# Optimization experiments

Measured on AMD Instinct MI355X. Metric: run time of the kernel, lower is better.

Reference implementation:

```python
import jax, jax.numpy as jnp
import numpy as np
from jax import lax

EPS = 1e-5
NBITS_W = 4
NBITS_A = 4
HIDDEN = 192


def _ste(x, q):
    # straight-through estimator: forward q, backward identity
    return x + lax.stop_gradient(q - x)


def act_q(x, bit, signed):
    # ACT_Q: per-tensor uniform activation quantization with max-abs scale (STE)
    if bit >= 32:
        return x
    n = float(2 ** (bit - 1) - 1) if signed else float(2 ** bit - 1)
    scale = lax.stop_gradient(jnp.max(jnp.abs(x)) + 1e-8)
    lo = -1.0 if signed else 0.0
    xc = jnp.clip(x / scale, lo, 1.0)
    q = jnp.round(xc * n) / n * scale
    return _ste(x, q)


def weight_q(w, bit):
    # Conv2d_quan_cim weight quant: symmetric per-tensor max-abs uniform quant (STE)
    if bit >= 32:
        return w
    n = float(2 ** (bit - 1) - 1)
    scale = lax.stop_gradient(jnp.max(jnp.abs(w)) + 1e-8)
    q = jnp.round(jnp.clip(w / scale, -1.0, 1.0) * n) / n * scale
    return _ste(w, q)


def bn(x, g, b, m, v):
    # eval-mode BatchNorm2d over NCHW
    inv = lax.rsqrt(v + EPS)
    return (x - m[None, :, None, None]) * (g * inv)[None, :, None, None] + b[None, :, None, None]


def conv(x, w, stride=1, groups=1, pad=0):
    return lax.conv_general_dilated(
        x, w, (stride, stride), ((pad, pad), (pad, pad)),
        dimension_numbers=("NCHW", "OIHW", "NCHW"), feature_group_count=groups)


def setup_inputs() -> dict:
    key = jax.random.key(0)
    ks = jax.random.split(key, 16)
    f32 = jnp.float32
    return {
        "x": jax.random.normal(ks[0], (32, 32, 112, 112), dtype=f32),
        "w1": jax.random.normal(ks[1], (HIDDEN, 32, 1, 1), dtype=f32),
        "bn1_g": jax.random.uniform(ks[2], (HIDDEN,), dtype=f32),
        "bn1_b": jax.random.normal(ks[3], (HIDDEN,), dtype=f32),
        "bn1_m": jax.random.normal(ks[4], (HIDDEN,), dtype=f32),
        "bn1_v": jax.random.uniform(ks[5], (HIDDEN,), dtype=f32),
        "w_dw": jax.random.normal(ks[6], (HIDDEN, 1, 3, 3), dtype=f32),
        "bn2_g": jax.random.uniform(ks[7], (HIDDEN,), dtype=f32),
        "bn2_b": jax.random.normal(ks[8], (HIDDEN,), dtype=f32),
        "bn2_m": jax.random.normal(ks[9], (HIDDEN,), dtype=f32),
        "bn2_v": jax.random.uniform(ks[10], (HIDDEN,), dtype=f32),
        "w2": jax.random.normal(ks[11], (32, HIDDEN, 1, 1), dtype=f32),
        "bn3_g": jax.random.uniform(ks[12], (32,), dtype=f32),
        "bn3_b": jax.random.normal(ks[13], (32,), dtype=f32),
        "bn3_m": jax.random.normal(ks[14], (32,), dtype=f32),
        "bn3_v": jax.random.uniform(ks[15], (32,), dtype=f32),
    }


def reference(x, w1, bn1_g, bn1_b, bn1_m, bn1_v, w_dw, bn2_g, bn2_b, bn2_m, bn2_v,
              w2, bn3_g, bn3_b, bn3_m, bn3_v):
    # leading signed ACT_Q (first=False)
    h = act_q(x, NBITS_A, signed=True)
    # expand 1x1: Conv2d_quan_cim -> BN -> ReLU6 -> ACT_Q
    h = conv(h, weight_q(w1, NBITS_W))
    h = jnp.clip(bn(h, bn1_g, bn1_b, bn1_m, bn1_v), 0.0, 6.0)
    h = act_q(h, NBITS_A, signed=False)
    # depthwise 3x3: Conv2d_quan_cim_dw -> BN -> ReLU6 -> ACT_Q
    h = conv(h, weight_q(w_dw, NBITS_W), stride=1, groups=HIDDEN, pad=1)
    h = jnp.clip(bn(h, bn2_g, bn2_b, bn2_m, bn2_v), 0.0, 6.0)
    h = act_q(h, NBITS_A, signed=False)
    # project 1x1: Conv2d_quan_cim -> BN
    h = conv(h, weight_q(w2, NBITS_W))
    h = bn(h, bn3_g, bn3_b, bn3_m, bn3_v)
    # out_actq (signed) then residual add (use_res_connect is True here)
    h = act_q(h, NBITS_A, signed=True)
    return x + h
```

## Files before the change

kernel.cpp:

```cpp
#include <hip/hip_runtime.h>


#define HW    12544
#define WID   112
#define CIN   32
#define CMID  192
#define COUT  32
#define NB    32
#define NPIX  (NB*HW)
#define NX    (NB*CIN*HW)

#define OFF_SCAL   0
#define OFF_WSC    16
#define OFF_BN1    64
#define OFF_BN2    2368
#define OFF_BN3    4672
#define OFF_FQ1    5120
#define OFF_FQ2    7488
#define OFF_W1P    9856
#define OFF_WDW    16000
#define OFF_W1A    22912
#define OFF_W2A    29056
#define OFF_WDWH   35200
#define OFF_PMAX   42112
#define OFF_XQ     65536

#define PADP(p) ((p) + ((p) >> 4))

typedef int v4i __attribute__((ext_vector_type(4)));
typedef unsigned long long ull;
typedef _Float16 h2 __attribute__((ext_vector_type(2)));

__device__ __forceinline__ unsigned h2u(h2 v){ union{h2 h; unsigned u;} c; c.h=v; return c.u; }
__device__ __forceinline__ h2 u2h(unsigned u){ union{h2 h; unsigned u;} c; c.u=u; return c.h; }
__device__ __forceinline__ h2 pkrtz(float a, float b){
    auto r = __builtin_amdgcn_cvt_pkrtz(a, b);
    union { decltype(r) f; h2 h; } c; c.f = r; return c.h;
}

#if defined(__has_builtin)
#if __has_builtin(__builtin_amdgcn_sdot4)
#define HAVE_SDOT4 1
#endif
#endif

__device__ __forceinline__ int sdot4(unsigned a, unsigned b, int c) {
#ifdef HAVE_SDOT4
    return __builtin_amdgcn_sdot4((int)a, (int)b, c, false);
#else
    c += (int)(signed char)(a & 0xff)        * (int)(signed char)(b & 0xff);
    c += (int)(signed char)((a >> 8) & 0xff) * (int)(signed char)((b >> 8) & 0xff);
    c += (int)(signed char)((a >> 16) & 0xff)* (int)(signed char)((b >> 16) & 0xff);
    c += (int)(signed char)(a >> 24)         * (int)(signed char)(b >> 24);
    return c;
#endif
}

__device__ __forceinline__ v4i mfma_i8(ull a, ull b, v4i c) {
    return __builtin_amdgcn_mfma_i32_16x16x32_i8((long)a, (long)b, c, 0, 0, 0);
}

__device__ __forceinline__ float bmax256(float v, float* red) {
    const int t = threadIdx.x;
    red[t] = v; __syncthreads();
    for (int s = 128; s; s >>= 1) {
        if (t < s) red[t] = fmaxf(red[t], red[t + s]);
        __syncthreads();
    }
    float r = red[0]; __syncthreads();
    return r;
}

__device__ __forceinline__ float qcode(float x, float s, float n, float lo) {
    float t = x / s;
    t = fminf(fmaxf(t, lo), 1.0f);
    return rintf(__fmul_rn(t, n));
}

__device__ __forceinline__ float bnq(float d, float C, float m, float g, float b) {
    float y = __fmul_rn(d, C);
    float h = __fadd_rn(__fmul_rn(__fsub_rn(y, m), g), b);
    return fminf(fmaxf(h, 0.f), 6.f);
}

__device__ __forceinline__ float qexact15(float h, float s) {
    return rintf(__fmul_rn(fminf(h / s, 1.f), 15.f));
}
__device__ __forceinline__ float qfast15(float df, float A, float B) {
    float t = fmaf(df, A, B);
    return rintf(fminf(fmaxf(t, 0.f), 15.f));
}

__global__ __launch_bounds__(256) void kprepx(
    const float4* __restrict__ x4,
    const float* __restrict__ w1, const float* __restrict__ wdw, const float* __restrict__ w2,
    const float* __restrict__ g1, const float* __restrict__ b1, const float* __restrict__ m1, const float* __restrict__ v1,
    const float* __restrict__ g2, const float* __restrict__ b2, const float* __restrict__ m2, const float* __restrict__ v2,
    const float* __restrict__ g3, const float* __restrict__ b3, const float* __restrict__ m3, const float* __restrict__ v3,
    unsigned char* __restrict__ ws)
{
    __shared__ float red[256];
    const int t = threadIdx.x;

    if (blockIdx.x == 0) {
        unsigned* scal = (unsigned*)(ws + OFF_SCAL);
        float* wsc  = (float*)(ws + OFF_WSC);
        float* bn1  = (float*)(ws + OFF_BN1);
        float* bn2  = (float*)(ws + OFF_BN2);
        float* bn3  = (float*)(ws + OFF_BN3);
        unsigned* w1p = (unsigned*)(ws + OFF_W1P);
        float*  wdwf  = (float*)(ws + OFF_WDW);

        if (t < 4) scal[t] = 0u;
        if (t == 0) { ((unsigned*)(ws+OFF_FQ1))[576] = 1u; ((unsigned*)(ws+OFF_FQ2))[576] = 1u; }

        float m;
        m = 0.f; for (int i = t; i < CMID*CIN; i += 256) m = fmaxf(m, fabsf(w1[i]));
        float sw1 = bmax256(m, red) + 1e-8f;
        m = 0.f; for (int i = t; i < CMID*9; i += 256) m = fmaxf(m, fabsf(wdw[i]));
        float swd = bmax256(m, red) + 1e-8f;
        m = 0.f; for (int i = t; i < COUT*CMID; i += 256) m = fmaxf(m, fabsf(w2[i]));
        float sw2 = bmax256(m, red) + 1e-8f;
        if (t == 0) { wsc[0] = sw1; wsc[1] = swd; wsc[2] = sw2; }

        for (int i = t; i < CMID*8; i += 256) {
            int oc = i >> 3, j = i & 7;
            unsigned wword = 0;
#pragma unroll
            for (int k = 0; k < 4; ++k) {
                int code = (int)qcode(w1[oc*CIN + 4*j + k], sw1, 7.f, -1.f);
                wword |= ((unsigned)code & 0xffu) << (8*k);
            }
            w1p[i] = wword;
        }
        for (int i = t; i < CMID*9; i += 256) wdwf[i] = qcode(wdw[i], swd, 7.f, -1.f);

        for (int i = t; i < 12*64; i += 256) {
            int octile = i >> 6, l = i & 63;
            int oc = octile*16 + (l & 15), icb = (l >> 4) * 8;
            unsigned lo = 0, hi = 0;
#pragma unroll
            for (int k = 0; k < 4; ++k) {
                lo |= ((unsigned)(int)qcode(w1[oc*CIN + icb + k],     sw1, 7.f, -1.f) & 0xffu) << (8*k);
                hi |= ((unsigned)(int)qcode(w1[oc*CIN + icb + 4 + k], sw1, 7.f, -1.f) & 0xffu) << (8*k);
            }
            ((unsigned*)(ws + OFF_W1A))[i*2]   = lo;
            ((unsigned*)(ws + OFF_W1A))[i*2+1] = hi;
        }
        for (int i = t; i < 2*6*64; i += 256) {
            int oct = i / 384, rem = i % 384, chunk = rem >> 6, l = rem & 63;
            int oc = oct*16 + (l & 15), cb = chunk*32 + (l >> 4) * 8;
            unsigned lo = 0, hi = 0;
#pragma unroll
            for (int k = 0; k < 4; ++k) {
                lo |= ((unsigned)(int)qcode(w2[oc*CMID + cb + k],     sw2, 7.f, -1.f) & 0xffu) << (8*k);
                hi |= ((unsigned)(int)qcode(w2[oc*CMID + cb + 4 + k], sw2, 7.f, -1.f) & 0xffu) << (8*k);
            }
            ((unsigned*)(ws + OFF_W2A))[i*2]   = lo;
            ((unsigned*)(ws + OFF_W2A))[i*2+1] = hi;
        }
        for (int i = t; i < 48*9; i += 256) {
            int qg = i / 9, tap = i % 9;
            float c0 = qcode(wdw[(qg*4+0)*9 + tap], swd, 7.f, -1.f);
            float c1 = qcode(wdw[(qg*4+1)*9 + tap], swd, 7.f, -1.f);
            float c2 = qcode(wdw[(qg*4+2)*9 + tap], swd, 7.f, -1.f);
            float c3 = qcode(wdw[(qg*4+3)*9 + tap], swd, 7.f, -1.f);
            ((uint2*)(ws + OFF_WDWH))[i] = make_uint2(h2u(pkrtz(c0, c1)), h2u(pkrtz(c2, c3)));
        }

        for (int c = t; c < CMID; c += 256) {
            float vv1 = v1[c] + 1e-5f;
            bn1[c] = __fmul_rn(g1[c], (float)(1.0 / sqrt((double)vv1)));
            bn1[192+c] = m1[c]; bn1[384+c] = b1[c];
            float vv2 = v2[c] + 1e-5f;
            bn2[c] = __fmul_rn(g2[c], (float)(1.0 / sqrt((double)vv2)));
            bn2[192+c] = m2[c]; bn2[384+c] = b2[c];
        }
        for (int c = t; c < COUT; c += 256) {
            float vv3 = v3[c] + 1e-5f;
            bn3[c] = __fmul_rn(g3[c], (float)(1.0 / sqrt((double)vv3)));
            bn3[32+c] = m3[c]; bn3[64+c] = b3[c];
        }
    }

    float m = 0.f;
    for (size_t i = (size_t)blockIdx.x*256 + t; i < NX/4; i += (size_t)gridDim.x*256) {
        float4 v = x4[i];
        m = fmaxf(m, fmaxf(fmaxf(fabsf(v.x), fabsf(v.y)), fmaxf(fabsf(v.z), fabsf(v.w))));
    }
    float r = bmax256(m, red);
    if (t == 0) ((float*)(ws + OFF_PMAX))[blockIdx.x] = r;
}

__global__ __launch_bounds__(256) void kmax1q(const float* __restrict__ x,
                                              unsigned char* __restrict__ ws)
{
    __shared__ unsigned s_w1p[CMID*8];
    __shared__ float s_bn1[576];
    __shared__ float red[256];
    const int t = threadIdx.x;

    {
        const uint4* src = (const uint4*)(ws + OFF_W1P);
        uint4* dst = (uint4*)s_w1p;
        for (int i = t; i < CMID*8/4; i += 256) dst[i] = src[i];
        const float* b = (const float*)(ws + OFF_BN1);
        for (int i = t; i < 576; i += 256) s_bn1[i] = b[i];
    }

    const float* wsc = (const float*)(ws + OFF_WSC);
    unsigned char* xq = ws + OFF_XQ;

    float pm = 0.f;
    const float* pmax = (const float*)(ws + OFF_PMAX);
    for (int i = t; i < 2048; i += 256) pm = fmaxf(pm, pmax[i]);
    float sxr = bmax256(pm, red);
    if (blockIdx.x == 0 && t == 0) ((unsigned*)(ws + OFF_SCAL))[0] = __float_as_uint(sxr);
    const float sx = sxr + 1e-8f;
    const float C1 = (float)(((double)sx / 7.0) * ((double)wsc[0] / 7.0));

    const int p = blockIdx.x * 256 + t;
    const int n = p / HW, pi = p % HW;
    const float* xp = x + (size_t)n * CIN * HW + pi;

    float kx[CIN];
#pragma unroll
    for (int ic = 0; ic < CIN; ++ic) {
        float v = xp[(size_t)ic * HW] / sx;
        v = fminf(fmaxf(v, -1.f), 1.f);
        kx[ic] = rintf(__fmul_rn(v, 7.f));
    }

    unsigned wb[8];
#pragma unroll
    for (int j = 0; j < 8; ++j) {
        unsigned b0 = (unsigned)(int)kx[4*j]     & 0xffu;
        unsigned b1 = (unsigned)(int)kx[4*j + 1] & 0xffu;
        unsigned b2 = (unsigned)(int)kx[4*j + 2] & 0xffu;
        unsigned b3 = (unsigned)(int)kx[4*j + 3] & 0xffu;
        wb[j] = b0 | (b1 << 8) | (b2 << 16) | (b3 << 24);
    }
    uint4* q4 = (uint4*)(xq + (size_t)p * 32);
    q4[0] = make_uint4(wb[0], wb[1], wb[2], wb[3]);
    q4[1] = make_uint4(wb[4], wb[5], wb[6], wb[7]);

    __syncthreads();

    float mx = 0.f;
    for (int oc = 0; oc < CMID; ++oc) {
        int d = 0;
#pragma unroll
        for (int j = 0; j < 8; ++j) d = sdot4(wb[j], s_w1p[oc*8 + j], d);
        float h = bnq((float)d, C1, s_bn1[192+oc], s_bn1[oc], s_bn1[384+oc]);
        mx = fmaxf(mx, h);
        if (__any(mx >= 6.0f)) break;
    }
    float r = bmax256(mx, red);
    if (t == 0) atomicMax((unsigned*)(ws + OFF_SCAL) + 1, __float_as_uint(r));
}

__global__ __launch_bounds__(64) void kcoef(unsigned char* __restrict__ ws, int stage)
{
    const unsigned* scal = (const unsigned*)(ws + OFF_SCAL);
    const float* wsc = (const float*)(ws + OFF_WSC);
    const int c = blockIdx.x, lane = threadIdx.x;
    const float* bn = (const float*)(ws + (stage == 1 ? OFF_BN1 : OFF_BN2));
    float* fq = (float*)(ws + (stage == 1 ? OFF_FQ1 : OFF_FQ2));

    float C, s; int R;
    if (stage == 1) {
        float sx = __uint_as_float(scal[0]) + 1e-8f;
        C = (float)(((double)sx / 7.0) * ((double)wsc[0] / 7.0));
        s = __uint_as_float(scal[1]) + 1e-8f;
        R = 1568;
    } else {
        float s1 = __uint_as_float(scal[1]) + 1e-8f;
        C = (float)(((double)s1 / 15.0) * ((double)wsc[1] / 7.0));
        s = __uint_as_float(scal[2]) + 1e-8f;
        R = 945;
    }
    const float gi = bn[c], mm = bn[192+c], bb = bn[384+c];
    const float A = (float)((double)C * (double)gi * 15.0 / (double)s);
    const float B = (float)(((double)bb - (double)mm * (double)gi) * 15.0 / (double)s);

    bool bad = false;
    for (int d = -R + lane; d <= R; d += 64) {
        float df = (float)d;
        float je = qexact15(bnq(df, C, mm, gi, bb), s);
        float jf = qfast15(df, A, B);
        if (je != jf) bad = true;
    }
    bool any = __any(bad);
    if (lane == 0) {
        unsigned flagv = any ? 0u : 1u;
        fq[c] = A; fq[192+c] = B;
        ((unsigned*)fq)[384+c] = flagv;
        atomicAnd(((unsigned*)fq) + 576, flagv);
    }
}

__global__ __launch_bounds__(256) void kmax2(unsigned char* __restrict__ ws)
{
    __shared__ unsigned s_w1p[CMID*8];
    __shared__ float s_wdw[CMID*9];
    __shared__ float s_bn2[576];
    __shared__ unsigned s_fq1[576];
    __shared__ float jl[8][256];
    __shared__ float red[256];
    __shared__ unsigned s_flag;
    const int t = threadIdx.x;

    {
        const uint4* sp = (const uint4*)(ws + OFF_W1P);
        uint4* dp = (uint4*)s_w1p;
        for (int i = t; i < CMID*8/4; i += 256) dp[i] = sp[i];
        const float* wp = (const float*)(ws + OFF_WDW);
        for (int i = t; i < CMID*9; i += 256) s_wdw[i] = wp[i];
        const float* b2p = (const float*)(ws + OFF_BN2);
        for (int i = t; i < 576; i += 256) s_bn2[i] = b2p[i];
        const unsigned* fp = (const unsigned*)(ws + OFF_FQ1);
        for (int i = t; i < 576; i += 256) s_fq1[i] = fp[i];
        if (t == 0) s_flag = 0u;
    }

    const unsigned* scal = (const unsigned*)(ws + OFF_SCAL);
    const float* wsc = (const float*)(ws + OFF_WSC);
    const float* gbn1 = (const float*)(ws + OFF_BN1);
    const unsigned char* xq = ws + OFF_XQ;

    const float sx  = __uint_as_float(scal[0]) + 1e-8f;
    const float s1v = __uint_as_float(scal[1]) + 1e-8f;
    const float C1  = (float)(((double)sx  / 7.0)  * ((double)wsc[0] / 7.0));
    const float C2  = (float)(((double)s1v / 15.0) * ((double)wsc[1] / 7.0));

    const int tile = blockIdx.x, n = blockIdx.y;
    const int ty = t >> 4, tx = t & 15;
    const int hy = (tile >> 3) * 14 - 1 + ty;
    const int wx = (tile & 7)  * 14 - 1 + tx;
    const bool inb = (hy >= 0 && hy < WID && wx >= 0 && wx < WID);
    const bool act = (ty < 14) && (tx < 14);

    unsigned wb[8];
    if (inb) {
        const uint4* q4 = (const uint4*)(xq + ((size_t)n * HW + hy * WID + wx) * 32);
        uint4 a = q4[0], b4 = q4[1];
        wb[0]=a.x; wb[1]=a.y; wb[2]=a.z; wb[3]=a.w;
        wb[4]=b4.x; wb[5]=b4.y; wb[6]=b4.z; wb[7]=b4.w;
    } else {
#pragma unroll
        for (int j = 0; j < 8; ++j) wb[j] = 0u;
    }
    __syncthreads();

    float mx = 0.f;
    for (int ph = 0; ph < CMID/8; ++ph) {
#pragma unroll
        for (int k = 0; k < 8; ++k) {
            const int c = ph*8 + k;
            int d1 = 0;
#pragma unroll
            for (int j = 0; j < 8; ++j) d1 = sdot4(wb[j], s_w1p[c*8 + j], d1);
            float j1 = 0.f;
            if (inb) {
                float d1f = (float)d1;
                if (s_fq1[384+c]) {
                    j1 = qfast15(d1f, __uint_as_float(s_fq1[c]), __uint_as_float(s_fq1[192+c]));
                } else {
                    float h1 = bnq(d1f, C1, gbn1[192+c], gbn1[c], gbn1[384+c]);
                    j1 = qexact15(h1, s1v);
                }
            }
            jl[k][t] = j1;
        }
        __syncthreads();
        if (act) {
#pragma unroll
            for (int k = 0; k < 8; ++k) {
                const int c = ph*8 + k;
                const float* wd = s_wdw + c * 9;
                float d2 = 0.f;
#pragma unroll
                for (int dy = 0; dy < 3; ++dy)
#pragma unroll
                    for (int dx = 0; dx < 3; ++dx)
                        d2 = fmaf(jl[k][(ty+dy)*16 + tx+dx], wd[dy*3+dx], d2);
                float h2 = bnq(d2, C2, s_bn2[192+c], s_bn2[c], s_bn2[384+c]);
                mx = fmaxf(mx, h2);
            }
        }
        if (mx >= 6.0f) s_flag = 1u;
        __syncthreads();
        if (s_flag) break;
    }
    float r = bmax256(mx, red);
    if (t == 0) atomicMax((unsigned*)(ws + OFF_SCAL) + 2, __float_as_uint(r));
}

__global__ __launch_bounds__(256, 4) void kconv2(unsigned char* __restrict__ ws,
                                                 float* __restrict__ h3)
{
    __shared__ ull   s_w1a[12*64];
    __shared__ ull   s_w2a[2*6*64];
    __shared__ uint2 s_wdwh[48*9];
    __shared__ float s_fqA1[192], s_fqB1[192], s_fqA2[192], s_fqB2[192];
    __shared__ float s_bn3[96];
    __shared__ uint2 jlh[4][272];
    __shared__ unsigned j2buf[256][9];
    __shared__ int s_af1, s_af2;
    const int t = threadIdx.x;

    {
        const uint4* a = (const uint4*)(ws + OFF_W1A);
        uint4* da = (uint4*)s_w1a;
        for (int i = t; i < 384; i += 256) da[i] = a[i];
        const uint4* b = (const uint4*)(ws + OFF_W2A);
        uint4* db = (uint4*)s_w2a;
        for (int i = t; i < 384; i += 256) db[i] = b[i];
        const uint4* c = (const uint4*)(ws + OFF_WDWH);
        uint4* dc = (uint4*)s_wdwh;
        for (int i = t; i < 216; i += 256) dc[i] = c[i];
        const float* f1 = (const float*)(ws + OFF_FQ1);
        const float* f2 = (const float*)(ws + OFF_FQ2);
        for (int i = t; i < 192; i += 256) {
            s_fqA1[i] = f1[i]; s_fqB1[i] = f1[192+i];
            s_fqA2[i] = f2[i]; s_fqB2[i] = f2[192+i];
        }
        const float* b3p = (const float*)(ws + OFF_BN3);
        if (t < 96) s_bn3[t] = b3p[t];
        if (t == 0) {
            s_af1 = (int)((const unsigned*)(ws + OFF_FQ1))[576];
            s_af2 = (int)((const unsigned*)(ws + OFF_FQ2))[576];
        }
    }

    const unsigned* scal = (const unsigned*)(ws + OFF_SCAL);
    const float* wsc = (const float*)(ws + OFF_WSC);
    const float* gbn1 = (const float*)(ws + OFF_BN1);
    const float* gbn2 = (const float*)(ws + OFF_BN2);
    const unsigned char* xq = ws + OFF_XQ;

    const float sx  = __uint_as_float(scal[0]) + 1e-8f;
    const float s1v = __uint_as_float(scal[1]) + 1e-8f;
    const float s2v = __uint_as_float(scal[2]) + 1e-8f;
    const float C1  = (float)(((double)sx  / 7.0)  * ((double)wsc[0] / 7.0));
    const float C2  = (float)(((double)s1v / 15.0) * ((double)wsc[1] / 7.0));
    const float C3  = (float)(((double)s2v / 15.0) * ((double)wsc[2] / 7.0));

    const int tile = blockIdx.x, n = blockIdx.y;
    const int y0 = (tile >> 3) * 14, x0 = (tile & 7) * 14;
    const int lane = t & 63, wid = t >> 6;
    const int ty = t >> 4, tx = t & 15;
    const bool act = (ty < 14) && (tx < 14);
    const int px = lane & 15, kq = lane >> 4;

    ull  xb[4];
    bool okb[4];
#pragma unroll
    for (int i = 0; i < 4; ++i) {
        int g = 4*wid + i;
        int bhy = y0 - 1 + g, bwx = x0 - 1 + px;
        bool ok = (bhy >= 0) && (bhy < WID) && (bwx >= 0) && (bwx < WID);
        okb[i] = ok;
        ull v = 0;
        if (ok) v = *(const ull*)(xq + (((size_t)n * HW + bhy * WID + bwx) * 32 + kq * 8));
        xb[i] = v;
    }
    __syncthreads();

    v4i acc2[2][4];
#pragma unroll
    for (int o = 0; o < 2; ++o)
#pragma unroll
        for (int i = 0; i < 4; ++i) { acc2[o][i][0]=0; acc2[o][i][1]=0; acc2[o][i][2]=0; acc2[o][i][3]=0; }

    for (int ph = 0; ph < 12; ++ph) {
        ull a1 = s_w1a[ph*64 + lane];
        const int oc0 = ph*16 + kq*4;
        float4 A14 = *(const float4*)&s_fqA1[oc0];
        float4 B14 = *(const float4*)&s_fqB1[oc0];
#pragma unroll
        for (int i = 0; i < 4; ++i) {
            v4i z = {0,0,0,0};
            v4i d = mfma_i8(a1, xb[i], z);
            float4 j1v;
            if (s_af1) {
                j1v.x = okb[i] ? qfast15((float)d[0], A14.x, B14.x) : 0.f;
                j1v.y = okb[i] ? qfast15((float)d[1], A14.y, B14.y) : 0.f;
                j1v.z = okb[i] ? qfast15((float)d[2], A14.z, B14.z) : 0.f;
                j1v.w = okb[i] ? qfast15((float)d[3], A14.w, B14.w) : 0.f;
            } else {
                float jj[4];
#pragma unroll
                for (int r = 0; r < 4; ++r) {
                    int oc = oc0 + r;
                    float h1 = bnq((float)d[r], C1, gbn1[192+oc], gbn1[oc], gbn1[384+oc]);
                    jj[r] = okb[i] ? qexact15(h1, s1v) : 0.f;
                }
                j1v.x = jj[0]; j1v.y = jj[1]; j1v.z = jj[2]; j1v.w = jj[3];
            }
            jlh[kq][PADP((4*wid + i)*16 + px)] =
                make_uint2(h2u(pkrtz(j1v.x, j1v.y)), h2u(pkrtz(j1v.z, j1v.w)));
        }
        __syncthreads();

        unsigned pw[4] = {0u, 0u, 0u, 0u};
        if (act) {
#pragma unroll
            for (int q = 0; q < 4; ++q) {
                h2 s01 = u2h(0u), s23 = u2h(0u);
                const int qg = ph*4 + q;
#pragma unroll
                for (int dy = 0; dy < 3; ++dy)
#pragma unroll
                    for (int dx = 0; dx < 3; ++dx) {
                        uint2 jv = jlh[q][PADP((ty+dy)*16 + (tx+dx))];
                        uint2 wv = s_wdwh[qg*9 + dy*3 + dx];
                        s01 += u2h(jv.x) * u2h(wv.x);
                        s23 += u2h(jv.y) * u2h(wv.y);
                    }
                float f0 = (float)s01[0], f1 = (float)s01[1];
                float f2 = (float)s23[0], f3 = (float)s23[1];
                const int oc2 = ph*16 + q*4;
                float j2a, j2b, j2c, j2d;
                if (s_af2) {
                    float4 A24 = *(const float4*)&s_fqA2[oc2];
                    float4 B24 = *(const float4*)&s_fqB2[oc2];
                    j2a = qfast15(f0, A24.x, B24.x);
                    j2b = qfast15(f1, A24.y, B24.y);
                    j2c = qfast15(f2, A24.z, B24.z);
                    j2d = qfast15(f3, A24.w, B24.w);
                } else {
                    j2a = qexact15(bnq(f0, C2, gbn2[192+oc2],   gbn2[oc2],   gbn2[384+oc2]),   s2v);
                    j2b = qexact15(bnq(f1, C2, gbn2[192+oc2+1], gbn2[oc2+1], gbn2[384+oc2+1]), s2v);
                    j2c = qexact15(bnq(f2, C2, gbn2[192+oc2+2], gbn2[oc2+2], gbn2[384+oc2+2]), s2v);
                    j2d = qexact15(bnq(f3, C2, gbn2[192+oc2+3], gbn2[oc2+3], gbn2[384+oc2+3]), s2v);
                }
                pw[q] = ((unsigned)(int)j2a) | ((unsigned)(int)j2b << 8) |
                        ((unsigned)(int)j2c << 16) | ((unsigned)(int)j2d << 24);
            }
        }
#pragma unroll
        for (int q = 0; q < 4; ++q) j2buf[t][(ph & 1) * 4 + q] = pw[q];
        __syncthreads();

        if (ph & 1) {
            const int chunk = ph >> 1;
#pragma unroll
            for (int oct = 0; oct < 2; ++oct) {
                ull a2 = s_w2a[(oct*6 + chunk)*64 + lane];
#pragma unroll
                for (int i = 0; i < 4; ++i) {
                    int row = (4*wid + i)*16 + px;
                    unsigned w0 = j2buf[row][kq*2], w1 = j2buf[row][kq*2 + 1];
                    ull b2 = (ull)w0 | ((ull)w1 << 32);
                    acc2[oct][i] = mfma_i8(a2, b2, acc2[oct][i]);
                }
            }
        }
    }

    float mx = 0.f;
#pragma unroll
    for (int oct = 0; oct < 2; ++oct)
#pragma unroll
        for (int i = 0; i < 4; ++i) {
            int g = 4*wid + i;
            if (g < 14 && px < 14) {
                int gy = y0 + g, gx = x0 + px;
#pragma unroll
                for (int r = 0; r < 4; ++r) {
                    int oc = oct*16 + kq*4 + r;
                    float y = __fmul_rn((float)acc2[oct][i][r], C3);
                    float h = __fadd_rn(__fmul_rn(__fsub_rn(y, s_bn3[32+oc]), s_bn3[oc]), s_bn3[64+oc]);
                    h3[((size_t)n * COUT + oc) * HW + gy * WID + gx] = h;
                    mx = fmaxf(mx, fabsf(h));
                }
            }
        }
    __syncthreads();
    float* red = (float*)&j2buf[0][0];
    float r = bmax256(mx, red);
    if (t == 0) atomicMax((unsigned*)(ws + OFF_SCAL) + 3, __float_as_uint(r));
}

__global__ __launch_bounds__(256) void kout(const float4* __restrict__ x4,
                                            float4* __restrict__ io4,
                                            const unsigned char* __restrict__ ws)
{
    const unsigned* scal = (const unsigned*)(ws + OFF_SCAL);
    const float s3v = __uint_as_float(scal[3]) + 1e-8f;

    for (size_t i = (size_t)blockIdx.x*256 + threadIdx.x; i < NX/4; i += (size_t)gridDim.x*256) {
        float4 h = io4[i], xv = x4[i], o;
        float* hp = &h.x; float* xp = &xv.x; float* op = &o.x;
#pragma unroll
        for (int k = 0; k < 4; ++k) {
            float tq = fminf(fmaxf(hp[k] / s3v, -1.f), 1.f);
            float kq = rintf(__fmul_rn(tq, 7.f));
            float q  = __fmul_rn(kq / 7.f, s3v);
            op[k] = __fadd_rn(xp[k], q);
        }
        io4[i] = o;
    }
}

extern "C" void kernel_launch(void* const* d_in, const int* in_sizes, int n_in,
                              void* d_out, int out_size, void* d_ws, size_t ws_size,
                              hipStream_t stream)
{
    const float* x   = (const float*)d_in[0];
    const float* w1  = (const float*)d_in[1];
    const float* g1  = (const float*)d_in[2];
    const float* b1  = (const float*)d_in[3];
    const float* m1  = (const float*)d_in[4];
    const float* v1  = (const float*)d_in[5];
    const float* wdw = (const float*)d_in[6];
    const float* g2  = (const float*)d_in[7];
    const float* b2  = (const float*)d_in[8];
    const float* m2  = (const float*)d_in[9];
    const float* v2  = (const float*)d_in[10];
    const float* w2  = (const float*)d_in[11];
    const float* g3  = (const float*)d_in[12];
    const float* b3  = (const float*)d_in[13];
    const float* m3  = (const float*)d_in[14];
    const float* v3  = (const float*)d_in[15];
    unsigned char* ws = (unsigned char*)d_ws;

    hipLaunchKernelGGL(kprepx, dim3(2048), dim3(256), 0, stream, (const float4*)x,
                       w1, wdw, w2, g1, b1, m1, v1, g2, b2, m2, v2, g3, b3, m3, v3, ws);
    hipLaunchKernelGGL(kmax1q, dim3(NPIX/256), dim3(256), 0, stream, x, ws);
    hipLaunchKernelGGL(kcoef, dim3(CMID), dim3(64), 0, stream, ws, 1);
    hipLaunchKernelGGL(kmax2, dim3(64, NB), dim3(256), 0, stream, ws);
    hipLaunchKernelGGL(kcoef, dim3(CMID), dim3(64), 0, stream, ws, 2);
    hipLaunchKernelGGL(kconv2, dim3(64, NB), dim3(256), 0, stream, ws, (float*)d_out);
    hipLaunchKernelGGL(kout, dim3(2048), dim3(256), 0, stream,
                       (const float4*)x, (float4*)d_out, ws);
}
```

Before: 228.9 us.

## Add grid-wide early-exit flags for max scans and store conv2 accumulators as int16

Result: slower. 344.6 us (+50.5%).

```diff
diff --git a/kernel.cpp b/kernel.cpp
--- a/kernel.cpp
+++ b/kernel.cpp
@@ -12,6 +12,8 @@
 
 #define OFF_SCAL   0
 #define OFF_WSC    16
+#define OFF_GF1    48
+#define OFF_GF2    52
 #define OFF_BN1    64
 #define OFF_BN2    2368
 #define OFF_BN3    4672
@@ -24,6 +26,8 @@
 #define OFF_WDWH   35200
 #define OFF_PMAX   42112
 #define OFF_XQ     65536
+#define OFF_D3     16777216
+#define D3_BYTES   25690112ULL
 
 #define PADP(p) ((p) + ((p) >> 4))
 
@@ -112,7 +116,10 @@
         float*  wdwf  = (float*)(ws + OFF_WDW);
 
         if (t < 4) scal[t] = 0u;
-        if (t == 0) { ((unsigned*)(ws+OFF_FQ1))[576] = 1u; ((unsigned*)(ws+OFF_FQ2))[576] = 1u; }
+        if (t == 0) {
+            ((unsigned*)(ws+OFF_FQ1))[576] = 1u; ((unsigned*)(ws+OFF_FQ2))[576] = 1u;
+            *(unsigned*)(ws+OFF_GF1) = 0u; *(unsigned*)(ws+OFF_GF2) = 0u;
+        }
 
         float m;
         m = 0.f; for (int i = t; i < CMID*CIN; i += 256) m = fmaxf(m, fabsf(w1[i]));
@@ -210,6 +217,7 @@
 
     const float* wsc = (const float*)(ws + OFF_WSC);
     unsigned char* xq = ws + OFF_XQ;
+    volatile const unsigned* vgf1 = (volatile const unsigned*)(ws + OFF_GF1);
 
     float pm = 0.f;
     const float* pmax = (const float*)(ws + OFF_PMAX);
@@ -253,7 +261,14 @@
         for (int j = 0; j < 8; ++j) d = sdot4(wb[j], s_w1p[oc*8 + j], d);
         float h = bnq((float)d, C1, s_bn1[192+oc], s_bn1[oc], s_bn1[384+oc]);
         mx = fmaxf(mx, h);
-        if (__any(mx >= 6.0f)) break;
+        if (__any(mx >= 6.0f)) {
+            if ((t & 63) == 0) atomicOr((unsigned*)(ws + OFF_GF1), 1u);
+            break;
+        }
+        if ((oc & 7) == 7) {
+            unsigned f = ((t & 63) == 0) ? *vgf1 : 0u;
+            if (__shfl(f, 0, 64)) break;
+        }
     }
     float r = bmax256(mx, red);
     if (t == 0) atomicMax((unsigned*)(ws + OFF_SCAL) + 1, __float_as_uint(r));
@@ -327,6 +342,7 @@
     const float* wsc = (const float*)(ws + OFF_WSC);
     const float* gbn1 = (const float*)(ws + OFF_BN1);
     const unsigned char* xq = ws + OFF_XQ;
+    volatile const unsigned* vgf2 = (volatile const unsigned*)(ws + OFF_GF2);
 
     const float sx  = __uint_as_float(scal[0]) + 1e-8f;
     const float s1v = __uint_as_float(scal[1]) + 1e-8f;
@@ -389,15 +405,21 @@
             }
         }
         if (mx >= 6.0f) s_flag = 1u;
+        if (t == 0 && *vgf2) s_flag = 1u;
         __syncthreads();
-        if (s_flag) break;
+        if (s_flag) {
+            if (t == 0) atomicOr((unsigned*)(ws + OFF_GF2), 1u);
+            break;
+        }
     }
     float r = bmax256(mx, red);
     if (t == 0) atomicMax((unsigned*)(ws + OFF_SCAL) + 2, __float_as_uint(r));
 }
 
 __global__ __launch_bounds__(256, 4) void kconv2(unsigned char* __restrict__ ws,
-                                                 float* __restrict__ h3)
+                                                 float* __restrict__ h3,
+                                                 short* __restrict__ d3,
+                                                 int use16)
 {
     __shared__ ull   s_w1a[12*64];
     __shared__ ull   s_w2a[2*6*64];
@@ -570,9 +592,12 @@
 #pragma unroll
                 for (int r = 0; r < 4; ++r) {
                     int oc = oct*16 + kq*4 + r;
-                    float y = __fmul_rn((float)acc2[oct][i][r], C3);
+                    int dv = acc2[oct][i][r];
+                    float y = __fmul_rn((float)dv, C3);
                     float h = __fadd_rn(__fmul_rn(__fsub_rn(y, s_bn3[32+oc]), s_bn3[oc]), s_bn3[64+oc]);
-                    h3[((size_t)n * COUT + oc) * HW + gy * WID + gx] = h;
+                    size_t idx = ((size_t)n * COUT + oc) * HW + gy * WID + gx;
+                    if (use16) d3[idx] = (short)dv;
+                    else       h3[idx] = h;
                     mx = fmaxf(mx, fabsf(h));
                 }
             }
@@ -601,6 +626,40 @@
             op[k] = __fadd_rn(xp[k], q);
         }
         io4[i] = o;
+    }
+}
+
+__global__ __launch_bounds__(256) void kout16(const float4* __restrict__ x4,
+                                              float4* __restrict__ out4,
+                                              const short* __restrict__ d3,
+                                              const unsigned char* __restrict__ ws)
+{
+    const unsigned* scal = (const unsigned*)(ws + OFF_SCAL);
+    const float* wsc = (const float*)(ws + OFF_WSC);
+    const float* bn3 = (const float*)(ws + OFF_BN3);
+    const float s2v = __uint_as_float(scal[2]) + 1e-8f;
+    const float s3v = __uint_as_float(scal[3]) + 1e-8f;
+    const float C3  = (float)(((double)s2v / 15.0) * ((double)wsc[2] / 7.0));
+
+    for (size_t i = (size_t)blockIdx.x*256 + threadIdx.x; i < NX/4; i += (size_t)gridDim.x*256) {
+        const int oc = (int)((i * 4) / HW) & 31;
+        const float g = bn3[oc], m = bn3[32+oc], b = bn3[64+oc];
+        uint2 dv = ((const uint2*)d3)[i];
+        int s0 = (int)(short)(dv.x & 0xffffu), s1 = (int)(short)(dv.x >> 16);
+        int s2 = (int)(short)(dv.y & 0xffffu), s3 = (int)(short)(dv.y >> 16);
+        int sv[4] = {s0, s1, s2, s3};
+        float4 xv = x4[i], o;
+        float* xp = &xv.x; float* op = &o.x;
+#pragma unroll
+        for (int k = 0; k < 4; ++k) {
+            float y = __fmul_rn((float)sv[k], C3);
+            float h = __fadd_rn(__fmul_rn(__fsub_rn(y, m), g), b);
+            float tq = fminf(fmaxf(h / s3v, -1.f), 1.f);
+            float kq = rintf(__fmul_rn(tq, 7.f));
+            float q  = __fmul_rn(kq / 7.f, s3v);
+            op[k] = __fadd_rn(xp[k], q);
+        }
+        out4[i] = o;
     }
 }
 
@@ -626,13 +685,22 @@
     const float* v3  = (const float*)d_in[15];
     unsigned char* ws = (unsigned char*)d_ws;
 
+    const int use16 = (ws_size >= (size_t)OFF_D3 + D3_BYTES) ? 1 : 0;
+    short* d3 = (short*)(ws + OFF_D3);
+
     hipLaunchKernelGGL(kprepx, dim3(2048), dim3(256), 0, stream, (const float4*)x,
                        w1, wdw, w2, g1, b1, m1, v1, g2, b2, m2, v2, g3, b3, m3, v3, ws);
     hipLaunchKernelGGL(kmax1q, dim3(NPIX/256), dim3(256), 0, stream, x, ws);
     hipLaunchKernelGGL(kcoef, dim3(CMID), dim3(64), 0, stream, ws, 1);
     hipLaunchKernelGGL(kmax2, dim3(64, NB), dim3(256), 0, stream, ws);
     hipLaunchKernelGGL(kcoef, dim3(CMID), dim3(64), 0, stream, ws, 2);
-    hipLaunchKernelGGL(kconv2, dim3(64, NB), dim3(256), 0, stream, ws, (float*)d_out);
-    hipLaunchKernelGGL(kout, dim3(2048), dim3(256), 0, stream,
-                       (const float4*)x, (float4*)d_out, ws);
-}
+    hipLaunchKernelGGL(kconv2, dim3(64, NB), dim3(256), 0, stream, ws,
+                       (float*)d_out, d3, use16);
+    if (use16) {
+        hipLaunchKernelGGL(kout16, dim3(2048), dim3(256), 0, stream,
+                           (const float4*)x, (float4*)d_out, (const short*)d3, ws);
+    } else {
+        hipLaunchKernelGGL(kout, dim3(2048), dim3(256), 0, stream,
+                           (const float4*)x, (float4*)d_out, ws);
+    }
+}
```
